# Kernel tuning notes

Hardware: AMD Instinct MI355X
Metric: run time of the kernel (lower is better)

Reference implementation:

```python
import jax, jax.numpy as jnp
import numpy as np

B, S, E, H, V = 16, 1024, 256, 256, 50257
BUDGET = 10  # percent of tokens kept


def setup_inputs() -> dict:
    key = jax.random.key(0)
    ks = jax.random.split(key, 11)
    scale = 0.05
    x = jax.random.randint(ks[0], (B, S), 0, V)
    lengths = jax.random.randint(ks[1], (B,), S // 2, S + 1)
    mask = jnp.arange(S)[None, :] < lengths[:, None]  # [B,S] bool, contiguous prefixes
    embed_table = jax.random.normal(ks[2], (V, E), dtype=jnp.float32) * scale
    w_ih_f = jax.random.normal(ks[3], (4 * H, E), dtype=jnp.float32) * scale
    w_hh_f = jax.random.normal(ks[4], (4 * H, H), dtype=jnp.float32) * scale
    b_f = jax.random.normal(ks[5], (4 * H,), dtype=jnp.float32) * scale
    w_ih_b = jax.random.normal(ks[6], (4 * H, E), dtype=jnp.float32) * scale
    w_hh_b = jax.random.normal(ks[7], (4 * H, H), dtype=jnp.float32) * scale
    b_b = jax.random.normal(ks[8], (4 * H,), dtype=jnp.float32) * scale
    z_w = jax.random.normal(ks[9], (2 * H,), dtype=jnp.float32) * scale
    z_b = jax.random.normal(ks[10], (), dtype=jnp.float32) * scale
    return dict(x=x, mask=mask, embed_table=embed_table,
                w_ih_f=w_ih_f, w_hh_f=w_hh_f, b_f=b_f,
                w_ih_b=w_ih_b, w_hh_b=w_hh_b, b_b=b_b,
                z_w=z_w, z_b=z_b)


def _lstm_dir(x_proj, w_hh, mask, reverse):
    """Masked unidirectional LSTM. x_proj: [B,S,4H] (input proj + bias precomputed).
    Mimics packed-sequence semantics: state frozen and output zeroed on padding."""
    xs = jnp.swapaxes(x_proj, 0, 1)                      # [S,B,4H]
    ms = jnp.swapaxes(mask, 0, 1)[..., None].astype(x_proj.dtype)  # [S,B,1]
    Hd = w_hh.shape[1]
    h0 = jnp.zeros((x_proj.shape[0], Hd), x_proj.dtype)

    def step(carry, inp):
        h, c = carry
        xp, m = inp
        gates = xp + h @ w_hh.T                          # [B,4H]
        i, f, g, o = jnp.split(gates, 4, axis=-1)        # torch gate order i,f,g,o
        i = jax.nn.sigmoid(i); f = jax.nn.sigmoid(f)
        g = jnp.tanh(g); o = jax.nn.sigmoid(o)
        c_new = f * c + i * g
        h_new = o * jnp.tanh(c_new)
        h = m * h_new + (1.0 - m) * h
        c = m * c_new + (1.0 - m) * c
        return (h, c), h * m

    _, hs = jax.lax.scan(step, (h0, h0), (xs, ms), reverse=reverse)
    return jnp.swapaxes(hs, 0, 1)                        # [B,S,H]


def reference(x, mask, embed_table, w_ih_f, w_hh_f, b_f, w_ih_b, w_hh_b, b_b, z_w, z_b):
    emb = embed_table[x]                                 # [B,S,E] (eval mode: dropout = id)
    xp_f = emb @ w_ih_f.T + b_f                          # precompute input projections
    xp_b = emb @ w_ih_b.T + b_b
    h_f = _lstm_dir(xp_f, w_hh_f, mask, reverse=False)
    h_b = _lstm_dir(xp_b, w_hh_b, mask, reverse=True)
    h = jnp.concatenate([h_f, h_b], axis=-1)             # [B,S,2H]
    # BernoulliGate: Linear(enc,1) -> sigmoid probs
    probs = jax.nn.sigmoid(h @ z_w + z_b)                # [B,S]
    lengths = mask.astype(jnp.int32).sum(1)              # [B]
    probs = jnp.where(mask, probs, 0.0)                  # z_probs[lengths:] = 0
    k = jnp.round(BUDGET / 100.0 * lengths.astype(jnp.float32)).astype(jnp.int32)  # per-sample budget
    # per-row top-k selection via rank (rank of each position under descending prob)
    ranks = jnp.argsort(jnp.argsort(-probs, axis=1), axis=1)
    z = ((ranks < k[:, None]) & (probs > 0)).astype(jnp.float32)
    z = jnp.where(mask, z, 0.0)
    return z
```

## Files before the change

### kernel.cpp

```cpp
#include <hip/hip_runtime.h>
#include <hip/hip_bf16.h>
#include <math.h>

#define BB 16
#define SS 1024
#define EE 256
#define HH 256
#define G4 1024

#define NCB 8
#define CBC 32
#define LTHR 512
#define NCLUST 32
#define CLW 256

static constexpr size_t HBUF_OFF = 0;
static constexpr size_t HBUF_BYTES = (size_t)2 * NCLUST * CLW * 8;
static constexpr size_t LEN_OFF  = 131072;
static constexpr size_t HIST_OFF = 139264;
static constexpr size_t XPF_OFF  = HIST_OFF + (size_t)2*BB*SS*HH*4;
static constexpr size_t XPB_OFF  = XPF_OFF + (size_t)BB*SS*G4*4;

__global__ void len_kernel(const void* __restrict__ mask, int* __restrict__ lengths)
{
    const int b = blockIdx.x;
    const int t = threadIdx.x;
    const unsigned char* mb = (const unsigned char*)mask;
    const bool byteFmt = (mb[1] != 0);
    int cnt = 0;
    if (byteFmt) {
        const unsigned char* row = mb + (size_t)b * SS;
        for (int i = t; i < SS; i += 256) cnt += (row[i] != 0);
    } else {
        const int* row = ((const int*)mask) + (size_t)b * SS;
        for (int i = t; i < SS; i += 256) cnt += (row[i] != 0);
    }
    __shared__ int sred[256];
    sred[t] = cnt;
    __syncthreads();
    for (int s = 128; s > 0; s >>= 1) { if (t < s) sred[t] += sred[t + s]; __syncthreads(); }
    if (t == 0) lengths[b] = sred[0];
}

#define GB_BM 128
#define GB_BN 128
#define GB_BK 32
__global__ __launch_bounds__(256) void xp_gemm(
    const int* __restrict__ x, const float* __restrict__ emb,
    const float* __restrict__ wf, const float* __restrict__ bf,
    const float* __restrict__ wb, const float* __restrict__ bb,
    float* __restrict__ xpF, float* __restrict__ xpB)
{
    __shared__ float As[GB_BK][GB_BM + 4];
    __shared__ float Bs[GB_BK][GB_BN + 4];
    __shared__ int idxs[GB_BM];

    const int t = threadIdx.x;
    const int tokBase = blockIdx.x * GB_BM;
    const int nBase   = blockIdx.y * GB_BN;
    const int nOff    = nBase & (G4 - 1);
    const float* Wp   = (nBase < G4) ? wf : wb;

    if (t < GB_BM) idxs[t] = x[tokBase + t];
    __syncthreads();

    const int tx = t & 15, ty = t >> 4;
    float acc[8][8];
#pragma unroll
    for (int i = 0; i < 8; i++)
#pragma unroll
        for (int j = 0; j < 8; j++) acc[i][j] = 0.f;

    for (int k0 = 0; k0 < EE; k0 += GB_BK) {
#pragma unroll
        for (int it = 0; it < 4; ++it) {
            const int flat = t + it * 256;
            const int m  = flat & 127;
            const int kq = flat >> 7;
            const int idx = idxs[m];
            const float4 av = *(const float4*)(emb + (size_t)idx * EE + k0 + kq * 4);
            As[kq * 4 + 0][m] = av.x; As[kq * 4 + 1][m] = av.y;
            As[kq * 4 + 2][m] = av.z; As[kq * 4 + 3][m] = av.w;
            const float4 bv = *(const float4*)(Wp + (size_t)(nOff + m) * EE + k0 + kq * 4);
            Bs[kq * 4 + 0][m] = bv.x; Bs[kq * 4 + 1][m] = bv.y;
            Bs[kq * 4 + 2][m] = bv.z; Bs[kq * 4 + 3][m] = bv.w;
        }
        __syncthreads();
#pragma unroll
        for (int k = 0; k < GB_BK; k++) {
            const float4 a0 = *(const float4*)&As[k][ty * 8];
            const float4 a1 = *(const float4*)&As[k][ty * 8 + 4];
            const float4 b0 = *(const float4*)&Bs[k][tx * 8];
            const float4 b1 = *(const float4*)&Bs[k][tx * 8 + 4];
            const float a_[8] = {a0.x, a0.y, a0.z, a0.w, a1.x, a1.y, a1.z, a1.w};
            const float b_[8] = {b0.x, b0.y, b0.z, b0.w, b1.x, b1.y, b1.z, b1.w};
#pragma unroll
            for (int i = 0; i < 8; i++)
#pragma unroll
                for (int j = 0; j < 8; j++) acc[i][j] = fmaf(a_[i], b_[j], acc[i][j]);
        }
        __syncthreads();
    }

    const float* biasP = (nBase < G4) ? bf : bb;
    float bj[8];
#pragma unroll
    for (int j = 0; j < 8; j++) bj[j] = biasP[nOff + tx * 8 + j];
    float* outP = (nBase < G4) ? xpF : xpB;
#pragma unroll
    for (int i = 0; i < 8; i++) {
        const int token = tokBase + ty * 8 + i;
        float* row = outP + (size_t)token * G4 + nOff + tx * 8;
        float4 v0, v1;
        v0.x = acc[i][0] + bj[0]; v0.y = acc[i][1] + bj[1];
        v0.z = acc[i][2] + bj[2]; v0.w = acc[i][3] + bj[3];
        v1.x = acc[i][4] + bj[4]; v1.y = acc[i][5] + bj[5];
        v1.z = acc[i][6] + bj[6]; v1.w = acc[i][7] + bj[7];
        *(float4*)row = v0;
        *(float4*)(row + 4) = v1;
    }
}

__global__ __launch_bounds__(LTHR) void lstm_kernel(
    const float* __restrict__ xpF, const float* __restrict__ xpB,
    const float* __restrict__ whhF, const float* __restrict__ whhB,
    const int* __restrict__ lengths,
    unsigned long long* __restrict__ hbuf,
    float* __restrict__ hist)
{
    const int bid     = blockIdx.x;
    const int cluster = bid & 31;
    const int cb      = bid >> 5;
    const int dir     = cluster & 1;
    const int smp     = cluster >> 1;
    const int t       = threadIdx.x;
    const int l       = t & 63;

    const float* xp  = dir ? xpB : xpF;
    const float* whh = dir ? whhB : whhF;

    const int row  = (t >> 6) * 16 + (l & 15);
    const int ks   = (l >> 4) & 3;
    const int gate = row >> 5;
    const int col  = row & 31;
    const int grow = gate * HH + cb * CBC + col;
    const bool ks0 = (ks == 0);
    const int jl = t & 31;

    __shared__ float h_stage[4][68];
    __shared__ float gates_s[128];

    float4 Wc[16];
    {
        const float4* wp = (const float4*)(whh + (size_t)grow * HH + ks * 64);
#pragma unroll
        for (int q = 0; q < 16; q++) Wc[q] = wp[q];
    }
    const int len = lengths[smp];
    float c_reg = 0.f, h_reg = 0.f;

    const unsigned long long* hRd0 = hbuf + cluster * CLW;
    const unsigned long long* hRd1 = hbuf + (size_t)NCLUST * CLW + cluster * CLW;
    unsigned long long* hWr0 = hbuf + cluster * CLW;
    unsigned long long* hWr1 = hbuf + (size_t)NCLUST * CLW + cluster * CLW;

    for (int n = 0; n < SS; ++n) {
        const int ts    = dir ? (SS - 1 - n) : n;
        const int par_r = (n + 1) & 1;
        const int par_w = n & 1;

        float xpv = 0.f;
        if (ks0) xpv = xp[((size_t)smp * SS + ts) * G4 + grow];

        if (t < 256) {
            const unsigned long long* src = (par_r ? hRd1 : hRd0) + t;
            unsigned long long v = __hip_atomic_load(src, __ATOMIC_RELAXED,
                                                     __HIP_MEMORY_SCOPE_AGENT);
            while ((unsigned int)(v >> 32) < (unsigned int)n) {
                __builtin_amdgcn_s_sleep(1);
                v = __hip_atomic_load(src, __ATOMIC_RELAXED,
                                      __HIP_MEMORY_SCOPE_AGENT);
            }
            h_stage[t >> 6][t & 63] = __builtin_bit_cast(float, (unsigned int)v);
        }
        __syncthreads();

        float a = 0.f;
        {
            const float4* hp = (const float4*)&h_stage[ks][0];
#pragma unroll
            for (int q = 0; q < 16; q++) {
                const float4 w4 = Wc[q], h4 = hp[q];
                a = fmaf(w4.x, h4.x, a); a = fmaf(w4.y, h4.y, a);
                a = fmaf(w4.z, h4.z, a); a = fmaf(w4.w, h4.w, a);
            }
        }
        a += __shfl_xor(a, 16);
        a += __shfl_xor(a, 32);
        if (ks0) {
            const float gv = a + xpv;
            gates_s[row] = (gate == 2) ? tanhf(gv) : 1.f / (1.f + expf(-gv));
        }
        __syncthreads();

        if (t < 32) {
            const float iv = gates_s[jl];
            const float fv = gates_s[32 + jl];
            const float gg = gates_s[64 + jl];
            const float ov = gates_s[96 + jl];
            const float cn = fmaf(fv, c_reg, iv * gg);
            const float hn = ov * tanhf(cn);
            const bool m = (ts < len);
            if (m) { c_reg = cn; h_reg = hn; }
            const unsigned long long val =
                (unsigned long long)__builtin_bit_cast(unsigned int, h_reg)
                | ((unsigned long long)(unsigned int)(n + 1) << 32);
            __hip_atomic_store((par_w ? hWr1 : hWr0) + cb * CBC + jl, val,
                               __ATOMIC_RELAXED, __HIP_MEMORY_SCOPE_AGENT);
            __builtin_nontemporal_store(m ? h_reg : 0.f,
                hist + (((size_t)dir * BB + smp) * SS + ts) * HH + cb * CBC + jl);
        }
    }
}

__global__ void out_kernel(const float* __restrict__ hist, const float* __restrict__ zw,
                           const float* __restrict__ zb, const int* __restrict__ lengths,
                           float* __restrict__ zout)
{
    const int b = blockIdx.x;
    const int t = threadIdx.x;
    __shared__ float probs[SS];
    __shared__ float zwsh[2 * HH];
    __shared__ int lsh;
    zwsh[t] = zw[t];
    zwsh[HH + t] = zw[HH + t];
    if (t == 0) lsh = lengths[b];
    __syncthreads();
    const int len = lsh;
    const float zbv = zb[0];

    for (int s = t; s < SS; s += 256) {
        const float4* hf  = (const float4*)(hist + ((size_t)b * SS + s) * HH);
        const float4* hb2 = (const float4*)(hist + (((size_t)BB + b) * SS + s) * HH);
        const float4* z0 = (const float4*)zwsh;
        const float4* z1 = (const float4*)(zwsh + HH);
        float acc = 0.f;
#pragma unroll 8
        for (int q = 0; q < HH / 4; q++) {
            const float4 h = hf[q], zv = z0[q];
            acc = fmaf(h.x, zv.x, acc); acc = fmaf(h.y, zv.y, acc);
            acc = fmaf(h.z, zv.z, acc); acc = fmaf(h.w, zv.w, acc);
        }
#pragma unroll 8
        for (int q = 0; q < HH / 4; q++) {
            const float4 h = hb2[q], zv = z1[q];
            acc = fmaf(h.x, zv.x, acc); acc = fmaf(h.y, zv.y, acc);
            acc = fmaf(h.z, zv.z, acc); acc = fmaf(h.w, zv.w, acc);
        }
        const float d = acc + zbv;
        probs[s] = (s < len) ? 1.f / (1.f + expf(-d)) : 0.f;
    }
    __syncthreads();

    const int kb = (int)rintf(0.1f * (float)len);
    for (int s = t; s < SS; s += 256) {
        const float p = probs[s];
        int rank = 0;
        for (int j = 0; j < SS; j++) {
            const float pj = probs[j];
            rank += (pj > p) ? 1 : 0;
            rank += ((pj == p) && (j < s)) ? 1 : 0;
        }
        zout[b * SS + s] = (s < len && rank < kb) ? 1.f : 0.f;
    }
}

extern "C" void kernel_launch(void* const* d_in, const int* in_sizes, int n_in,
                              void* d_out, int out_size, void* d_ws, size_t ws_size,
                              hipStream_t stream)
{
    (void)in_sizes; (void)n_in; (void)out_size; (void)ws_size;
    const int*   x    = (const int*)d_in[0];
    const void*  mask = d_in[1];
    const float* emb  = (const float*)d_in[2];
    const float* wihf = (const float*)d_in[3];
    const float* whhf = (const float*)d_in[4];
    const float* bf   = (const float*)d_in[5];
    const float* wihb = (const float*)d_in[6];
    const float* whhb = (const float*)d_in[7];
    const float* bb   = (const float*)d_in[8];
    const float* zw   = (const float*)d_in[9];
    const float* zb   = (const float*)d_in[10];
    float* zout = (float*)d_out;

    char* ws = (char*)d_ws;
    unsigned long long* hbuf = (unsigned long long*)(ws + HBUF_OFF);
    int*   lengths           = (int*)(ws + LEN_OFF);
    float* hist              = (float*)(ws + HIST_OFF);
    float* xpF               = (float*)(ws + XPF_OFF);
    float* xpB               = (float*)(ws + XPB_OFF);

    hipMemsetAsync(ws, 0, HBUF_BYTES, stream);

    len_kernel<<<BB, 256, 0, stream>>>(mask, lengths);
    xp_gemm<<<dim3((BB * SS) / GB_BM, (2 * G4) / GB_BN), 256, 0, stream>>>(
        x, emb, wihf, bf, wihb, bb, xpF, xpB);
    lstm_kernel<<<NCB * NCLUST, LTHR, 0, stream>>>(xpF, xpB, whhf, whhb, lengths,
                                                   hbuf, hist);
    out_kernel<<<BB, 256, 0, stream>>>(hist, zw, zb, lengths, zout);
}
```

Baseline: 1.873 ms.

## Remove second barrier in LSTM step via wave-local gate shuffles; split rank kernel

Remaps LSTM threads so each wavefront holds all four gates for four hidden units. The gate activations are exchanged with __shfl instead of shared memory, which removes the second __syncthreads per timestep. h_stage is double-buffered by parity so the single remaining barrier is enough. The out_kernel is split across 4 blocks per sample to parallelize the O(S^2) rank computation, at the cost of recomputing probs redundantly in each block.

```diff
diff --git a/kernel.cpp b/kernel.cpp
--- a/kernel.cpp
+++ b/kernel.cpp
@@ -121,7 +121,7 @@
     }
 }
 
-__global__ __launch_bounds__(LTHR) void lstm_kernel(
+__global__ __launch_bounds__(LTHR, 2) void lstm_kernel(
     const float* __restrict__ xpF, const float* __restrict__ xpB,
     const float* __restrict__ whhF, const float* __restrict__ whhB,
     const int* __restrict__ lengths,
@@ -134,21 +134,20 @@
     const int dir     = cluster & 1;
     const int smp     = cluster >> 1;
     const int t       = threadIdx.x;
+    const int w       = t >> 6;
     const int l       = t & 63;
 
     const float* xp  = dir ? xpB : xpF;
     const float* whh = dir ? whhB : whhF;
 
-    const int row  = (t >> 6) * 16 + (l & 15);
-    const int ks   = (l >> 4) & 3;
-    const int gate = row >> 5;
-    const int col  = row & 31;
-    const int grow = gate * HH + cb * CBC + col;
+    const int ks   = l >> 4;
+    const int gate = (l >> 2) & 3;
+    const int cq   = l & 3;
+    const int jloc = w * 4 + cq;
+    const int grow = gate * HH + cb * CBC + jloc;
     const bool ks0 = (ks == 0);
-    const int jl = t & 31;
-
-    __shared__ float h_stage[4][68];
-    __shared__ float gates_s[128];
+
+    __shared__ float h_stage[2][4][68];
 
     float4 Wc[16];
     {
@@ -156,6 +155,10 @@
 #pragma unroll
         for (int q = 0; q < 16; q++) Wc[q] = wp[q];
     }
+#pragma unroll
+    for (int q = 0; q < 16; q++)
+        asm volatile("" : "+v"(Wc[q].x), "+v"(Wc[q].y), "+v"(Wc[q].z), "+v"(Wc[q].w));
+
     const int len = lengths[smp];
     float c_reg = 0.f, h_reg = 0.f;
 
@@ -181,13 +184,13 @@
                 v = __hip_atomic_load(src, __ATOMIC_RELAXED,
                                       __HIP_MEMORY_SCOPE_AGENT);
             }
-            h_stage[t >> 6][t & 63] = __builtin_bit_cast(float, (unsigned int)v);
+            h_stage[par_r][t >> 6][t & 63] = __builtin_bit_cast(float, (unsigned int)v);
         }
         __syncthreads();
 
         float a = 0.f;
         {
-            const float4* hp = (const float4*)&h_stage[ks][0];
+            const float4* hp = (const float4*)&h_stage[par_r][ks][0];
 #pragma unroll
             for (int q = 0; q < 16; q++) {
                 const float4 w4 = Wc[q], h4 = hp[q];
@@ -197,17 +200,16 @@
         }
         a += __shfl_xor(a, 16);
         a += __shfl_xor(a, 32);
-        if (ks0) {
-            const float gv = a + xpv;
-            gates_s[row] = (gate == 2) ? tanhf(gv) : 1.f / (1.f + expf(-gv));
-        }
-        __syncthreads();
-
-        if (t < 32) {
-            const float iv = gates_s[jl];
-            const float fv = gates_s[32 + jl];
-            const float gg = gates_s[64 + jl];
-            const float ov = gates_s[96 + jl];
+
+        const float gv  = a + xpv;
+        const float act = (gate == 2) ? tanhf(gv) : 1.f / (1.f + expf(-gv));
+
+        const float iv = __shfl(act, cq);
+        const float fv = __shfl(act, 4 + cq);
+        const float gg = __shfl(act, 8 + cq);
+        const float ov = __shfl(act, 12 + cq);
+
+        if (l < 4) {
             const float cn = fmaf(fv, c_reg, iv * gg);
             const float hn = ov * tanhf(cn);
             const bool m = (ts < len);
@@ -215,10 +217,10 @@
             const unsigned long long val =
                 (unsigned long long)__builtin_bit_cast(unsigned int, h_reg)
                 | ((unsigned long long)(unsigned int)(n + 1) << 32);
-            __hip_atomic_store((par_w ? hWr1 : hWr0) + cb * CBC + jl, val,
+            __hip_atomic_store((par_w ? hWr1 : hWr0) + cb * CBC + jloc, val,
                                __ATOMIC_RELAXED, __HIP_MEMORY_SCOPE_AGENT);
             __builtin_nontemporal_store(m ? h_reg : 0.f,
-                hist + (((size_t)dir * BB + smp) * SS + ts) * HH + cb * CBC + jl);
+                hist + (((size_t)dir * BB + smp) * SS + ts) * HH + cb * CBC + jloc);
         }
     }
 }
@@ -227,8 +229,9 @@
                            const float* __restrict__ zb, const int* __restrict__ lengths,
                            float* __restrict__ zout)
 {
-    const int b = blockIdx.x;
-    const int t = threadIdx.x;
+    const int b    = blockIdx.x;
+    const int quad = blockIdx.y;
+    const int t    = threadIdx.x;
     __shared__ float probs[SS];
     __shared__ float zwsh[2 * HH];
     __shared__ int lsh;
@@ -263,16 +266,15 @@
     __syncthreads();
 
     const int kb = (int)rintf(0.1f * (float)len);
-    for (int s = t; s < SS; s += 256) {
-        const float p = probs[s];
-        int rank = 0;
-        for (int j = 0; j < SS; j++) {
-            const float pj = probs[j];
-            rank += (pj > p) ? 1 : 0;
-            rank += ((pj == p) && (j < s)) ? 1 : 0;
-        }
-        zout[b * SS + s] = (s < len && rank < kb) ? 1.f : 0.f;
-    }
+    const int s = quad * 256 + t;
+    const float p = probs[s];
+    int rank = 0;
+    for (int j = 0; j < SS; j++) {
+        const float pj = probs[j];
+        rank += (pj > p) ? 1 : 0;
+        rank += ((pj == p) && (j < s)) ? 1 : 0;
+    }
+    zout[b * SS + s] = (s < len && rank < kb) ? 1.f : 0.f;
 }
 
 extern "C" void kernel_launch(void* const* d_in, const int* in_sizes, int n_in,
@@ -307,5 +309,5 @@
         x, emb, wihf, bf, wihb, bb, xpF, xpB);
     lstm_kernel<<<NCB * NCLUST, LTHR, 0, stream>>>(xpF, xpB, whhf, whhb, lengths,
                                                    hbuf, hist);
-    out_kernel<<<BB, 256, 0, stream>>>(hist, zw, zb, lengths, zout);
-}
+    out_kernel<<<dim3(BB, 4), 256, 0, stream>>>(hist, zw, zb, lengths, zout);
+}
```

New measurement: 3.294 ms. 75.8% more time.
